# Performance work log

Hardware: AMD Instinct MI355X
Metric: run time of the kernel (lower is better)

Reference implementation:

```python
import jax, jax.numpy as jnp
import numpy as np

NUM_GRAPHS = 256
BN_EPS = 1e-5
GN_EPS = 1e-5


def setup_inputs() -> dict:
    key = jax.random.key(0)
    ks = jax.random.split(key, 8)
    N, E, D, H = 100000, 600000, 128, 128
    x = jax.random.normal(ks[0], (N, D), dtype=jnp.float32)
    W1 = jax.random.normal(ks[1], (4, 4 * H, D), dtype=jnp.float32) * 0.05
    bn_g = jnp.ones((4, 4 * H), dtype=jnp.float32)
    bn_b = jnp.zeros((4, 4 * H), dtype=jnp.float32)
    W2 = jax.random.normal(ks[2], (4, H, 4 * H), dtype=jnp.float32) * 0.05
    b2 = jnp.zeros((4, H), dtype=jnp.float32)
    gn_g = jnp.ones((4, H), dtype=jnp.float32)
    gn_b = jnp.zeros((4, H), dtype=jnp.float32)
    gn_a = jnp.ones((4, H), dtype=jnp.float32)
    edge_index = jax.random.randint(ks[3], (2, E), 0, N, dtype=jnp.int64)
    batch = jnp.sort(jax.random.randint(ks[4], (N,), 0, NUM_GRAPHS, dtype=jnp.int64))
    return {"x": x, "W1": W1, "bn_g": bn_g, "bn_b": bn_b, "W2": W2, "b2": b2,
            "gn_g": gn_g, "gn_b": gn_b, "gn_a": gn_a,
            "edge_index": edge_index, "batch": batch}


def reference(x, W1, bn_g, bn_b, W2, b2, gn_g, gn_b, gn_a, edge_index, batch):
    N = x.shape[0]
    src, dst = edge_index[0], edge_index[1]
    # per-graph node counts (shared by GraphNorm and mean-pool)
    cnt = jax.ops.segment_sum(jnp.ones((N,), x.dtype), batch, num_segments=NUM_GRAPHS)
    cnt = jnp.maximum(cnt, 1.0)[:, None]  # [G,1]

    h = x
    hs = []
    for l in range(4):  # fixed small layer loop
        # GINConv: (1+eps)*x + sum_{j->i} x_j, eps=0 default
        agg = jax.ops.segment_sum(h[src], dst, num_segments=N)
        z = h + agg
        # MLP: Linear(no bias) -> BatchNorm1d (batch stats) -> SELU -> Linear
        z = z @ W1[l].T
        mu = jnp.mean(z, axis=0)
        var = jnp.mean((z - mu) ** 2, axis=0)
        z = (z - mu) * jax.lax.rsqrt(var + BN_EPS) * bn_g[l] + bn_b[l]
        z = jax.nn.selu(z)
        z = z @ W2[l].T + b2[l]
        # GraphNorm: per-graph mean/var with learnable mean scale alpha
        gmean = jax.ops.segment_sum(z, batch, num_segments=NUM_GRAPHS) / cnt
        sub = z - gn_a[l] * gmean[batch]
        gvar = jax.ops.segment_sum(sub * sub, batch, num_segments=NUM_GRAPHS) / cnt
        z = gn_g[l] * sub * jax.lax.rsqrt(gvar[batch] + GN_EPS) + gn_b[l]
        z = jax.nn.selu(z)  # self.act (SELU, matching MLP)
        hs.append(z)
        h = z

    hg = jnp.concatenate(hs, axis=1)  # [N, 4*H]
    pooled = jax.ops.segment_sum(hg, batch, num_segments=NUM_GRAPHS) / cnt
    return pooled
```

## Files before the change

### kernel.cpp

```cpp
#include <hip/hip_runtime.h>
#include <hip/hip_bf16.h>


typedef __attribute__((ext_vector_type(8))) short bf16x8;
typedef __attribute__((ext_vector_type(4))) float f32x4;

#define MOMB 256

__device__ __forceinline__ unsigned short f2b(float x){
    __hip_bfloat16 h = __float2bfloat16(x);
    return *reinterpret_cast<unsigned short*>(&h);
}
__device__ __forceinline__ float b2f(unsigned short u){
    __hip_bfloat16 h;
    *reinterpret_cast<unsigned short*>(&h) = u;
    return __bfloat162float(h);
}
__device__ __forceinline__ float selu_f(float x){
    const float sc = 1.0507009873554805f, al = 1.6732632423543772f;
    return x > 0.f ? sc * x : sc * al * (__expf(x) - 1.f);
}

__global__ void count_kernel(const int* __restrict__ dst, int* __restrict__ counts, int E){
    int e = blockIdx.x * 256 + threadIdx.x;
    if (e < E) atomicAdd(&counts[dst[e]], 1);
}

__global__ void cnt_bs_kernel(const int* __restrict__ batch, float* __restrict__ cnt, int N){
    __shared__ int sb[257];
    int g = threadIdx.x;
    int lo = 0, hi = N;
    while (lo < hi){ int mid = (lo + hi) >> 1; if (batch[mid] < g) lo = mid + 1; else hi = mid; }
    sb[g] = lo;
    if (g == 0) sb[256] = N;
    __syncthreads();
    cnt[g] = fmaxf((float)(sb[g + 1] - sb[g]), 1.f);
}

__global__ __launch_bounds__(1024) void scan_kernel(const int* __restrict__ counts,
                                                    int* __restrict__ row_ptr, int N){
    __shared__ int wsum[16];
    __shared__ int wpre[16];
    __shared__ int s_total;
    __shared__ int s_running;
    int tid = threadIdx.x;
    int lane = tid & 63, wid = tid >> 6;
    if (tid == 0) s_running = 0;
    __syncthreads();
    for (int base = 0; base < N; base += 4096){
        int idx0 = base + tid * 4;
        int v[4];
        #pragma unroll
        for (int j = 0; j < 4; j++) v[j] = (idx0 + j < N) ? counts[idx0 + j] : 0;
        int tsum = v[0] + v[1] + v[2] + v[3];
        int x = tsum;
        #pragma unroll
        for (int off = 1; off < 64; off <<= 1){
            int y = __shfl_up(x, off, 64);
            if (lane >= off) x += y;
        }
        if (lane == 63) wsum[wid] = x;
        __syncthreads();
        if (wid == 0 && lane < 16){
            int w = wsum[lane];
            int xx = w;
            #pragma unroll
            for (int off = 1; off < 16; off <<= 1){
                int y = __shfl_up(xx, off, 64);
                if (lane >= off) xx += y;
            }
            wpre[lane] = xx - w;
            if (lane == 15) s_total = xx;
        }
        __syncthreads();
        int run = s_running + wpre[wid] + (x - tsum);
        #pragma unroll
        for (int j = 0; j < 4; j++){
            if (idx0 + j < N) row_ptr[idx0 + j] = run;
            run += v[j];
        }
        __syncthreads();
        if (tid == 0) s_running += s_total;
        __syncthreads();
    }
    if (tid == 0) row_ptr[N] = s_running;
}

__global__ void fill_kernel(const int* __restrict__ ei, const int* __restrict__ row_ptr,
                            int* __restrict__ fill, int* __restrict__ colv, int E){
    int e = blockIdx.x * 256 + threadIdx.x;
    if (e < E){
        int s = ei[e];
        int d = ei[E + e];
        int pos = atomicAdd(&fill[d], 1);
        colv[row_ptr[d] + pos] = s;
    }
}

__global__ void pack_kernel(const float* __restrict__ W1, const float* __restrict__ W2,
                            unsigned short* __restrict__ W1p, unsigned short* __restrict__ W2p){
    int t = blockIdx.x * 256 + threadIdx.x;
    int which = t >> 15;
    int u = t & 32767;
    int lane = u & 63; u >>= 6;
    int nf = u & 3; u >>= 2;
    int wc = u & 1; u >>= 1;
    int kk = u & 3; u >>= 2;
    int c = u & 3; u >>= 2;
    int l = u;
    int col = wc * 64 + nf * 16 + (lane & 15);
    int kbase = kk * 32 + (lane >> 4) * 8;
    size_t ob = ((((((size_t)(l * 4 + c) * 4 + kk) * 2 + wc) * 4 + nf) * 2) * 512) + lane * 8;
    unsigned short* dst = which == 0 ? W1p : W2p;
    #pragma unroll
    for (int j = 0; j < 8; j++){
        int k = kbase + j;
        float wv = which == 0 ? W1[((size_t)(l * 512) + c * 128 + col) * 128 + k]
                              : W2[((size_t)(l * 128) + col) * 512 + c * 128 + k];
        unsigned short hi = f2b(wv);
        unsigned short lo = f2b(wv - b2f(hi));
        dst[ob + j] = hi;
        dst[ob + 512 + j] = lo;
    }
}

__global__ __launch_bounds__(256) void agg_split_kernel(
    const float* __restrict__ h, const int* __restrict__ row_ptr,
    const int* __restrict__ colv,
    unsigned short* __restrict__ zhi, unsigned short* __restrict__ zlo, int N)
{
    int t = blockIdx.x * 256 + threadIdx.x;
    int i = t >> 5;
    if (i >= N) return;
    int vo = (t & 31);
    const float4* hv = reinterpret_cast<const float4*>(h);
    int p0 = row_ptr[i], p1 = row_ptr[i + 1];
    float4 acc = hv[(size_t)i * 32 + vo];
    int p = p0;
    for (; p + 4 <= p1; p += 4){
        int s0 = colv[p], s1 = colv[p + 1], s2 = colv[p + 2], s3 = colv[p + 3];
        float4 a = hv[(size_t)s0 * 32 + vo];
        float4 b = hv[(size_t)s1 * 32 + vo];
        float4 c = hv[(size_t)s2 * 32 + vo];
        float4 d = hv[(size_t)s3 * 32 + vo];
        acc.x += (a.x + b.x) + (c.x + d.x);
        acc.y += (a.y + b.y) + (c.y + d.y);
        acc.z += (a.z + b.z) + (c.z + d.z);
        acc.w += (a.w + b.w) + (c.w + d.w);
    }
    for (; p < p1; p++){
        float4 a = hv[(size_t)colv[p] * 32 + vo];
        acc.x += a.x; acc.y += a.y; acc.z += a.z; acc.w += a.w;
    }
    float vals[4] = {acc.x, acc.y, acc.z, acc.w};
    unsigned int h01, h23, l01, l23;
    {
        unsigned short hh[4], ll[4];
        #pragma unroll
        for (int j = 0; j < 4; j++){
            hh[j] = f2b(vals[j]);
            ll[j] = f2b(vals[j] - b2f(hh[j]));
        }
        h01 = (unsigned int)hh[0] | ((unsigned int)hh[1] << 16);
        h23 = (unsigned int)hh[2] | ((unsigned int)hh[3] << 16);
        l01 = (unsigned int)ll[0] | ((unsigned int)ll[1] << 16);
        l23 = (unsigned int)ll[2] | ((unsigned int)ll[3] << 16);
    }
    int kk = vo >> 3, kg = (vo >> 1) & 3, half = vo & 1;
    size_t fo = ((size_t)(i >> 4) * 4 + kk) * 512 + (kg * 16 + (i & 15)) * 8 + half * 4;
    *reinterpret_cast<uint2*>(zhi + fo) = make_uint2(h01, h23);
    *reinterpret_cast<uint2*>(zlo + fo) = make_uint2(l01, l23);
}

__device__ __forceinline__ bf16x8 tread(const unsigned short* __restrict__ s, int base){
    union { bf16x8 v; unsigned short u[8]; } r;
    #pragma unroll
    for (int j = 0; j < 8; j++) r.u[j] = s[base + j * 8];
    return r.v;
}

__global__ __launch_bounds__(256) void moment_k(
    const unsigned short* __restrict__ Zhi_g, const unsigned short* __restrict__ Zlo_g,
    float* __restrict__ Mpart, float* __restrict__ cpart, int RB)
{
    __shared__ __align__(16) unsigned short Zh_s[16384];
    __shared__ __align__(16) unsigned short Zl_s[16384];
    __shared__ float cs[256];
    int tid = threadIdx.x, lane = tid & 63, w = tid >> 6;
    int fl = lane & 15, g = lane >> 4;
    int tpart = (g >> 1) * 2048 + (g & 1) * 64;
    int fpart = (fl >> 3) * 128 + (fl & 7);

    f32x4 acc[2][8];
    #pragma unroll
    for (int i = 0; i < 2; i++)
        #pragma unroll
        for (int j = 0; j < 8; j++) acc[i][j] = (f32x4){0.f, 0.f, 0.f, 0.f};
    float csum = 0.f;
    int cf = tid & 127, chalf = tid >> 7;
    int cfbase = (cf >> 5) * 512 + ((cf >> 3) & 3) * 128 + (cf & 7);

    for (int blk = blockIdx.x; blk < RB; blk += MOMB){
        __syncthreads();
        {
            size_t gbase = (size_t)blk * 16384;
            const uint4* gh = reinterpret_cast<const uint4*>(Zhi_g + gbase);
            const uint4* gl = reinterpret_cast<const uint4*>(Zlo_g + gbase);
            uint4* sh4 = reinterpret_cast<uint4*>(Zh_s);
            uint4* sl4 = reinterpret_cast<uint4*>(Zl_s);
            #pragma unroll
            for (int j = 0; j < 8; j++){
                sh4[j * 256 + tid] = gh[j * 256 + tid];
                sl4[j * 256 + tid] = gl[j * 256 + tid];
            }
        }
        __syncthreads();

        #pragma unroll 8
        for (int n = chalf * 64; n < chalf * 64 + 64; n++){
            int addr = (n >> 4) * 2048 + (n & 15) * 8 + cfbase;
            csum += b2f(Zh_s[addr]) + b2f(Zl_s[addr]);
        }

        for (int nk = 0; nk < 4; nk++){
            int nb = nk * 4096 + tpart + fpart;
            bf16x8 ath[2], atl[2];
            #pragma unroll
            for (int i = 0; i < 2; i++){
                int ft = w * 2 + i;
                int base = nb + (ft >> 1) * 512 + (ft & 1) * 256;
                ath[i] = tread(Zh_s, base);
                atl[i] = tread(Zl_s, base);
            }
            #pragma unroll
            for (int ft2 = 0; ft2 < 8; ft2++){
                int base2 = nb + (ft2 >> 1) * 512 + (ft2 & 1) * 256;
                bf16x8 bth = tread(Zh_s, base2);
                bf16x8 btl = tread(Zl_s, base2);
                #pragma unroll
                for (int i = 0; i < 2; i++){
                    acc[i][ft2] = __builtin_amdgcn_mfma_f32_16x16x32_bf16(ath[i], bth, acc[i][ft2], 0, 0, 0);
                    acc[i][ft2] = __builtin_amdgcn_mfma_f32_16x16x32_bf16(ath[i], btl, acc[i][ft2], 0, 0, 0);
                    acc[i][ft2] = __builtin_amdgcn_mfma_f32_16x16x32_bf16(atl[i], bth, acc[i][ft2], 0, 0, 0);
                }
            }
        }
    }

    float* Mp = Mpart + (size_t)blockIdx.x * 16384;
    int col = lane & 15, rbase = (lane >> 4) * 4;
    #pragma unroll
    for (int i = 0; i < 2; i++)
        #pragma unroll
        for (int ft2 = 0; ft2 < 8; ft2++)
            #pragma unroll
            for (int r = 0; r < 4; r++){
                int a = (w * 2 + i) * 16 + rbase + r;
                int b = ft2 * 16 + col;
                Mp[a * 128 + b] = acc[i][ft2][r];
            }
    cs[tid] = csum;
    __syncthreads();
    if (tid < 128) cpart[(size_t)blockIdx.x * 128 + tid] = cs[tid] + cs[tid + 128];
}

__global__ __launch_bounds__(256) void reduce_k(
    const float* __restrict__ Mpart, const float* __restrict__ cpart,
    float* __restrict__ Msum, float* __restrict__ colsum)
{
    int gid = blockIdx.x * 256 + threadIdx.x;
    float s = 0.f;
    for (int p = 0; p < MOMB; p++) s += Mpart[(size_t)p * 16384 + gid];
    Msum[gid] = s;
    if (blockIdx.x == 0 && threadIdx.x < 128){
        float c = 0.f;
        for (int p = 0; p < MOMB; p++) c += cpart[(size_t)p * 128 + threadIdx.x];
        colsum[threadIdx.x] = c;
    }
}

__global__ __launch_bounds__(128) void bn_final2_k(
    const float* __restrict__ Msum, const float* __restrict__ colsum,
    const float* __restrict__ W1, const float* __restrict__ bng,
    const float* __restrict__ bnb, float* __restrict__ sc, float* __restrict__ sh,
    int l, float invN)
{
    __shared__ float s_w[128];
    __shared__ float red[4];
    int j = blockIdx.x;
    int t = threadIdx.x;
    float wt = W1[(size_t)l * 65536 + (size_t)j * 128 + t];
    s_w[t] = wt;
    __syncthreads();
    float y = 0.f;
    #pragma unroll 4
    for (int k = 0; k < 128; k++) y = fmaf(Msum[t * 128 + k], s_w[k], y);
    float p = wt * y;
    float mc = wt * colsum[t];
    #pragma unroll
    for (int off = 32; off >= 1; off >>= 1){
        p += __shfl_xor(p, off, 64);
        mc += __shfl_xor(mc, off, 64);
    }
    int lane = t & 63, wv = t >> 6;
    if (lane == 0){ red[wv * 2] = p; red[wv * 2 + 1] = mc; }
    __syncthreads();
    if (t == 0){
        float e2 = (red[0] + red[2]) * invN;
        float mu = (red[1] + red[3]) * invN;
        float var = e2 - mu * mu;
        float inv = rsqrtf(var + 1e-5f);
        float gg = bng[l * 512 + j] * inv;
        sc[j] = gg;
        sh[j] = bnb[l * 512 + j] - mu * gg;
    }
}

__global__ __launch_bounds__(512, 1) void fused_k(
    const unsigned short* __restrict__ Zhi_g, const unsigned short* __restrict__ Zlo_g,
    const unsigned short* __restrict__ B1p, const unsigned short* __restrict__ B2p,
    float* __restrict__ Z, const float* __restrict__ bsc, const float* __restrict__ bsh,
    const float* __restrict__ b2l, int N)
{
    __shared__ __align__(16) unsigned short Zh_s[16384];
    __shared__ __align__(16) unsigned short Zl_s[16384];
    __shared__ __align__(16) unsigned short Ph[128][136];
    __shared__ __align__(16) unsigned short Pl[128][136];
    __shared__ float s_sc[512], s_sh[512];
    int tid = threadIdx.x, lane = tid & 63, w = tid >> 6;
    int wr = w >> 2, wq = w & 3;
    int r_lo = lane & 15, kg = lane >> 4;
    int m0 = blockIdx.x * 128;

    if (tid < 512){ s_sc[tid] = bsc[tid]; s_sh[tid] = bsh[tid]; }
    {
        size_t gbase = (size_t)(m0 >> 4) * 2048;
        const uint4* gh = reinterpret_cast<const uint4*>(Zhi_g + gbase);
        const uint4* gl = reinterpret_cast<const uint4*>(Zlo_g + gbase);
        uint4* sh4 = reinterpret_cast<uint4*>(Zh_s);
        uint4* sl4 = reinterpret_cast<uint4*>(Zl_s);
        #pragma unroll
        for (int j = 0; j < 4; j++){
            sh4[j * 512 + tid] = gh[j * 512 + tid];
            sl4[j * 512 + tid] = gl[j * 512 + tid];
        }
    }
    __syncthreads();

    int wc = wq >> 1;
    f32x4 acc2[4][2];
    #pragma unroll
    for (int i = 0; i < 4; i++)
        #pragma unroll
        for (int j = 0; j < 2; j++) acc2[i][j] = (f32x4){0.f, 0.f, 0.f, 0.f};

    for (int c = 0; c < 4; c++){
        f32x4 acc1[2][4];
        #pragma unroll
        for (int i = 0; i < 2; i++)
            #pragma unroll
            for (int j = 0; j < 4; j++) acc1[i][j] = (f32x4){0.f, 0.f, 0.f, 0.f};

        const bf16x8* B1v = reinterpret_cast<const bf16x8*>(B1p) + (size_t)c * 4096;
        for (int kk = 0; kk < 4; kk++){
            bf16x8 awh[2], awl[2];
            #pragma unroll
            for (int mfp = 0; mfp < 2; mfp++){
                int colblk = wq * 2 + mfp;
                int wc1 = colblk >> 2, nf1 = colblk & 3;
                int ob = ((kk * 2 + wc1) * 4 + nf1) * 2;
                awh[mfp] = B1v[(ob + 0) * 64 + lane];
                awl[mfp] = B1v[(ob + 1) * 64 + lane];
            }
            bf16x8 bzh[4], bzl[4];
            #pragma unroll
            for (int nfp = 0; nfp < 4; nfp++){
                int so = ((wr * 4 + nfp) * 4 + kk) * 512 + lane * 8;
                bzh[nfp] = *reinterpret_cast<const bf16x8*>(&Zh_s[so]);
                bzl[nfp] = *reinterpret_cast<const bf16x8*>(&Zl_s[so]);
            }
            #pragma unroll
            for (int mfp = 0; mfp < 2; mfp++)
                #pragma unroll
                for (int nfp = 0; nfp < 4; nfp++){
                    acc1[mfp][nfp] = __builtin_amdgcn_mfma_f32_16x16x32_bf16(awh[mfp], bzh[nfp], acc1[mfp][nfp], 0, 0, 0);
                    acc1[mfp][nfp] = __builtin_amdgcn_mfma_f32_16x16x32_bf16(awh[mfp], bzl[nfp], acc1[mfp][nfp], 0, 0, 0);
                    acc1[mfp][nfp] = __builtin_amdgcn_mfma_f32_16x16x32_bf16(awl[mfp], bzh[nfp], acc1[mfp][nfp], 0, 0, 0);
                }
        }

        __syncthreads();
        #pragma unroll
        for (int mfp = 0; mfp < 2; mfp++){
            int ckb = wq * 32 + mfp * 16 + kg * 4;
            float sc0 = s_sc[c * 128 + ckb + 0], sh0 = s_sh[c * 128 + ckb + 0];
            float sc1 = s_sc[c * 128 + ckb + 1], sh1 = s_sh[c * 128 + ckb + 1];
            float sc2 = s_sc[c * 128 + ckb + 2], sh2 = s_sh[c * 128 + ckb + 2];
            float sc3 = s_sc[c * 128 + ckb + 3], sh3 = s_sh[c * 128 + ckb + 3];
            #pragma unroll
            for (int nfp = 0; nfp < 4; nfp++){
                float t0 = selu_f(fmaf(acc1[mfp][nfp][0], sc0, sh0));
                float t1 = selu_f(fmaf(acc1[mfp][nfp][1], sc1, sh1));
                float t2 = selu_f(fmaf(acc1[mfp][nfp][2], sc2, sh2));
                float t3 = selu_f(fmaf(acc1[mfp][nfp][3], sc3, sh3));
                unsigned short h0 = f2b(t0), h1 = f2b(t1), h2 = f2b(t2), h3 = f2b(t3);
                unsigned short l0 = f2b(t0 - b2f(h0)), l1 = f2b(t1 - b2f(h1));
                unsigned short l2 = f2b(t2 - b2f(h2)), l3 = f2b(t3 - b2f(h3));
                int node = wr * 64 + nfp * 16 + r_lo;
                uint2 hv = make_uint2((unsigned int)h0 | ((unsigned int)h1 << 16),
                                      (unsigned int)h2 | ((unsigned int)h3 << 16));
                uint2 lv = make_uint2((unsigned int)l0 | ((unsigned int)l1 << 16),
                                      (unsigned int)l2 | ((unsigned int)l3 << 16));
                *reinterpret_cast<uint2*>(&Ph[node][ckb]) = hv;
                *reinterpret_cast<uint2*>(&Pl[node][ckb]) = lv;
            }
        }
        __syncthreads();

        const bf16x8* B2v = reinterpret_cast<const bf16x8*>(B2p);
        for (int kk2 = 0; kk2 < 4; kk2++){
            int kkf = c * 4 + kk2;
            bf16x8 bh[2], bl[2];
            #pragma unroll
            for (int nf = 0; nf < 2; nf++){
                int nfold = (wq & 1) * 2 + nf;
                int ob = ((kkf * 2 + wc) * 4 + nfold) * 2;
                bh[nf] = B2v[(ob + 0) * 64 + lane];
                bl[nf] = B2v[(ob + 1) * 64 + lane];
            }
            bf16x8 ah[4], alr[4];
            #pragma unroll
            for (int mf = 0; mf < 4; mf++){
                int ar = wr * 64 + mf * 16 + r_lo;
                ah[mf]  = *reinterpret_cast<const bf16x8*>(&Ph[ar][kk2 * 32 + kg * 8]);
                alr[mf] = *reinterpret_cast<const bf16x8*>(&Pl[ar][kk2 * 32 + kg * 8]);
            }
            #pragma unroll
            for (int mf = 0; mf < 4; mf++)
                #pragma unroll
                for (int nf = 0; nf < 2; nf++){
                    acc2[mf][nf] = __builtin_amdgcn_mfma_f32_16x16x32_bf16(ah[mf],  bh[nf], acc2[mf][nf], 0, 0, 0);
                    acc2[mf][nf] = __builtin_amdgcn_mfma_f32_16x16x32_bf16(ah[mf],  bl[nf], acc2[mf][nf], 0, 0, 0);
                    acc2[mf][nf] = __builtin_amdgcn_mfma_f32_16x16x32_bf16(alr[mf], bh[nf], acc2[mf][nf], 0, 0, 0);
                }
        }
    }

    #pragma unroll
    for (int nf = 0; nf < 2; nf++){
        int col = wq * 32 + nf * 16 + r_lo;
        float bv = b2l[col];
        #pragma unroll
        for (int mf = 0; mf < 4; mf++)
            #pragma unroll
            for (int r = 0; r < 4; r++){
                int row = m0 + wr * 64 + mf * 16 + kg * 4 + r;
                if (row < N)
                    Z[(size_t)row * 128 + col] = bv + acc2[mf][nf][r];
            }
    }
}

__global__ __launch_bounds__(256) void gn_stats_kernel(
    const float* __restrict__ z2, const int* __restrict__ batch,
    float* __restrict__ gsum, float* __restrict__ gsq, int N)
{
    __shared__ int sb[128];
    int tid = threadIdx.x;
    int base = blockIdx.x * 128;
    int end = min(128, N - base);
    if (tid < 128) sb[tid] = (tid < end) ? batch[base + tid] : 0;
    __syncthreads();
    int vo = tid & 31;
    int r0 = (tid >> 5) * 16;
    if (r0 >= end) return;
    int rend = min(r0 + 16, end);
    const float4* zv = reinterpret_cast<const float4*>(z2);
    float sx = 0.f, sy = 0.f, sz = 0.f, sw = 0.f;
    float qx = 0.f, qy = 0.f, qz = 0.f, qw = 0.f;
    int run_g = sb[r0];
    for (int r = r0; r < rend; r++){
        int g = sb[r];
        if (g != run_g){
            float* gs = &gsum[run_g * 128 + vo * 4];
            float* gq = &gsq[run_g * 128 + vo * 4];
            atomicAdd(gs + 0, sx); atomicAdd(gs + 1, sy); atomicAdd(gs + 2, sz); atomicAdd(gs + 3, sw);
            atomicAdd(gq + 0, qx); atomicAdd(gq + 1, qy); atomicAdd(gq + 2, qz); atomicAdd(gq + 3, qw);
            sx = sy = sz = sw = 0.f; qx = qy = qz = qw = 0.f;
            run_g = g;
        }
        float4 v = zv[(size_t)(base + r) * 32 + vo];
        sx += v.x; sy += v.y; sz += v.z; sw += v.w;
        qx += v.x * v.x; qy += v.y * v.y; qz += v.z * v.z; qw += v.w * v.w;
    }
    float* gs = &gsum[run_g * 128 + vo * 4];
    float* gq = &gsq[run_g * 128 + vo * 4];
    atomicAdd(gs + 0, sx); atomicAdd(gs + 1, sy); atomicAdd(gs + 2, sz); atomicAdd(gs + 3, sw);
    atomicAdd(gq + 0, qx); atomicAdd(gq + 1, qy); atomicAdd(gq + 2, qz); atomicAdd(gq + 3, qw);
}

__global__ void gn_final_kernel(float* __restrict__ gsum, float* __restrict__ gsq,
                                const float* __restrict__ cnt,
                                const float* __restrict__ gng, const float* __restrict__ gnb,
                                const float* __restrict__ gna,
                                float* __restrict__ scale, float* __restrict__ shift, int l){
    int g = blockIdx.x, c = threadIdx.x;
    int idx = g * 128 + c;
    float n = cnt[g];
    float m = gsum[idx] / n;
    float e2 = gsq[idx] / n;
    float a = gna[l * 128 + c];
    float var = e2 - (2.f * a - a * a) * m * m;
    float inv = rsqrtf(var + 1e-5f);
    float sc = gng[l * 128 + c] * inv;
    scale[idx] = sc;
    shift[idx] = gnb[l * 128 + c] - a * m * sc;
    gsum[idx] = 0.f;
    gsq[idx] = 0.f;
}

__global__ __launch_bounds__(256) void gn_apply_kernel(
    float* __restrict__ z2h, const int* __restrict__ batch,
    const float* __restrict__ scale, const float* __restrict__ shift,
    float* __restrict__ pool, int l, int N)
{
    __shared__ int sb[128];
    int tid = threadIdx.x;
    int base = blockIdx.x * 128;
    int end = min(128, N - base);
    if (tid < 128) sb[tid] = (tid < end) ? batch[base + tid] : 0;
    __syncthreads();
    int vo = tid & 31;
    int r0 = (tid >> 5) * 16;
    if (r0 >= end) return;
    int rend = min(r0 + 16, end);
    float4* zv = reinterpret_cast<float4*>(z2h);
    int run_g = sb[r0];
    float scx = scale[run_g * 128 + vo * 4 + 0], shx = shift[run_g * 128 + vo * 4 + 0];
    float scy = scale[run_g * 128 + vo * 4 + 1], shy = shift[run_g * 128 + vo * 4 + 1];
    float scz = scale[run_g * 128 + vo * 4 + 2], shz = shift[run_g * 128 + vo * 4 + 2];
    float scw = scale[run_g * 128 + vo * 4 + 3], shw = shift[run_g * 128 + vo * 4 + 3];
    float px = 0.f, py = 0.f, pz = 0.f, pw = 0.f;
    for (int r = r0; r < rend; r++){
        int g = sb[r];
        if (g != run_g){
            float* pp = &pool[run_g * 512 + l * 128 + vo * 4];
            atomicAdd(pp + 0, px); atomicAdd(pp + 1, py); atomicAdd(pp + 2, pz); atomicAdd(pp + 3, pw);
            px = py = pz = pw = 0.f;
            run_g = g;
            scx = scale[g * 128 + vo * 4 + 0]; shx = shift[g * 128 + vo * 4 + 0];
            scy = scale[g * 128 + vo * 4 + 1]; shy = shift[g * 128 + vo * 4 + 1];
            scz = scale[g * 128 + vo * 4 + 2]; shz = shift[g * 128 + vo * 4 + 2];
            scw = scale[g * 128 + vo * 4 + 3]; shw = shift[g * 128 + vo * 4 + 3];
        }
        size_t idx = (size_t)(base + r) * 32 + vo;
        float4 v = zv[idx];
        v.x = selu_f(fmaf(v.x, scx, shx));
        v.y = selu_f(fmaf(v.y, scy, shy));
        v.z = selu_f(fmaf(v.z, scz, shz));
        v.w = selu_f(fmaf(v.w, scw, shw));
        zv[idx] = v;
        px += v.x; py += v.y; pz += v.z; pw += v.w;
    }
    float* pp = &pool[run_g * 512 + l * 128 + vo * 4];
    atomicAdd(pp + 0, px); atomicAdd(pp + 1, py); atomicAdd(pp + 2, pz); atomicAdd(pp + 3, pw);
}

__global__ void final_kernel(const float* __restrict__ pool, const float* __restrict__ cnt,
                             float* __restrict__ out, int n){
    int i = blockIdx.x * 256 + threadIdx.x;
    if (i < n) out[i] = pool[i] / cnt[i >> 9];
}

extern "C" void kernel_launch(void* const* d_in, const int* in_sizes, int n_in,
                              void* d_out, int out_size, void* d_ws, size_t ws_size,
                              hipStream_t stream){
    const float* x    = (const float*)d_in[0];
    const float* W1   = (const float*)d_in[1];
    const float* bng  = (const float*)d_in[2];
    const float* bnb  = (const float*)d_in[3];
    const float* W2   = (const float*)d_in[4];
    const float* b2   = (const float*)d_in[5];
    const float* gng  = (const float*)d_in[6];
    const float* gnb  = (const float*)d_in[7];
    const float* gna  = (const float*)d_in[8];
    const int*   ei   = (const int*)d_in[9];
    const int*   batch= (const int*)d_in[10];
    int N = in_sizes[0] / 128;
    int E = in_sizes[9] / 2;
    float* out = (float*)d_out;
    int RB = (N + 127) / 128;

    char* ws = (char*)d_ws;
    size_t off = 0;
    auto alloc = [&](size_t bytes) -> char* {
        char* p = ws + off;
        off += (bytes + 255) & ~(size_t)255;
        return p;
    };
    unsigned short* z0hi = (unsigned short*)alloc((size_t)RB * 128 * 128 * 2);
    unsigned short* z0lo = (unsigned short*)alloc((size_t)RB * 128 * 128 * 2);
    float* z2     = (float*)alloc((size_t)N * 128 * 4);
    unsigned short* W1p = (unsigned short*)alloc(524288 * 2);
    unsigned short* W2p = (unsigned short*)alloc(524288 * 2);
    int*   row_ptr= (int*)alloc((size_t)(N + 1) * 4);
    int*   colv   = (int*)alloc((size_t)E * 4);
    int*   counts = (int*)alloc((size_t)N * 4);
    int*   fill   = (int*)alloc((size_t)N * 4);
    float* cnt_f  = (float*)alloc(256 * 4);
    float* Mpart  = (float*)alloc((size_t)MOMB * 16384 * 4);
    float* cpart  = (float*)alloc((size_t)MOMB * 128 * 4);
    float* Msum   = (float*)alloc(16384 * 4);
    float* colsum = (float*)alloc(128 * 4);
    float* bn_sc  = (float*)alloc(512 * 4);
    float* bn_sh  = (float*)alloc(512 * 4);
    float* gn_sum = (float*)alloc(256 * 128 * 4);
    float* gn_sq  = (float*)alloc(256 * 128 * 4);
    float* gn_sc  = (float*)alloc(256 * 128 * 4);
    float* gn_sh  = (float*)alloc(256 * 128 * 4);
    float* pool   = (float*)alloc(256 * 512 * 4);
    (void)ws_size;

    hipMemsetAsync(counts, 0, (size_t)N * 4, stream);
    hipMemsetAsync(fill,   0, (size_t)N * 4, stream);
    hipMemsetAsync(gn_sum, 0, 2 * 256 * 128 * 4, stream);
    hipMemsetAsync(pool,   0, 256 * 512 * 4, stream);
    {
        size_t tail_start = (size_t)(N >> 4) * 2048;
        size_t total      = (size_t)RB * 128 * 128;
        if (total > tail_start){
            size_t tail_bytes = (total - tail_start) * 2;
            hipMemsetAsync(z0hi + tail_start, 0, tail_bytes, stream);
            hipMemsetAsync(z0lo + tail_start, 0, tail_bytes, stream);
        }
    }

    pack_kernel<<<256, 256, 0, stream>>>(W1, W2, W1p, W2p);
    count_kernel<<<(E + 255) / 256, 256, 0, stream>>>(ei + E, counts, E);
    scan_kernel<<<1, 1024, 0, stream>>>(counts, row_ptr, N);
    fill_kernel<<<(E + 255) / 256, 256, 0, stream>>>(ei, row_ptr, fill, colv, E);
    cnt_bs_kernel<<<1, 256, 0, stream>>>(batch, cnt_f, N);

    const float* hcur = x;
    float invN = 1.f / (float)N;
    for (int l = 0; l < 4; l++){
        agg_split_kernel<<<(N + 7) / 8, 256, 0, stream>>>(hcur, row_ptr, colv, z0hi, z0lo, N);
        moment_k<<<MOMB, 256, 0, stream>>>(z0hi, z0lo, Mpart, cpart, RB);
        reduce_k<<<64, 256, 0, stream>>>(Mpart, cpart, Msum, colsum);
        bn_final2_k<<<512, 128, 0, stream>>>(Msum, colsum, W1, bng, bnb,
                                             bn_sc, bn_sh, l, invN);
        fused_k<<<RB, 512, 0, stream>>>(z0hi, z0lo, W1p + (size_t)l * 131072,
                                        W2p + (size_t)l * 131072, z2,
                                        bn_sc, bn_sh, b2 + l * 128, N);
        gn_stats_kernel<<<RB, 256, 0, stream>>>(z2, batch, gn_sum, gn_sq, N);
        gn_final_kernel<<<256, 128, 0, stream>>>(gn_sum, gn_sq, cnt_f, gng, gnb, gna,
                                                 gn_sc, gn_sh, l);
        gn_apply_kernel<<<RB, 256, 0, stream>>>(z2, batch, gn_sc, gn_sh, pool, l, N);
        hcur = z2;
    }
    final_kernel<<<(out_size + 255) / 256, 256, 0, stream>>>(pool, cnt_f, out, out_size);
}
```

Baseline: 1.475 ms.

## Fuse GraphNorm stats into fused MLP kernel and use 1024-thread blocks

Removes the separate gn_stats kernel by accumulating per-graph sum and sum-of-squares in the fused MLP epilogue, using run-length segments over the sorted batch ids, which saves re-reading z2 from memory. It also doubles the block to 1024 threads (16 waves), halving each wave's node tile so per-thread accumulator registers drop. The tradeoff is more atomics: each output column now issues them per small run instead of per larger run. Register pressure under launch_bounds(1024,1) may also cause spills.

```diff
diff --git a/kernel.cpp b/kernel.cpp
--- a/kernel.cpp
+++ b/kernel.cpp
@@ -316,23 +316,26 @@
     }
 }
 
-__global__ __launch_bounds__(512, 1) void fused_k(
+__global__ __launch_bounds__(1024, 1) void fused_k(
     const unsigned short* __restrict__ Zhi_g, const unsigned short* __restrict__ Zlo_g,
     const unsigned short* __restrict__ B1p, const unsigned short* __restrict__ B2p,
     float* __restrict__ Z, const float* __restrict__ bsc, const float* __restrict__ bsh,
-    const float* __restrict__ b2l, int N)
+    const float* __restrict__ b2l, const int* __restrict__ batch,
+    float* __restrict__ gsum, float* __restrict__ gsq, int N)
 {
     __shared__ __align__(16) unsigned short Zh_s[16384];
     __shared__ __align__(16) unsigned short Zl_s[16384];
     __shared__ __align__(16) unsigned short Ph[128][136];
     __shared__ __align__(16) unsigned short Pl[128][136];
     __shared__ float s_sc[512], s_sh[512];
+    __shared__ int s_b[128];
     int tid = threadIdx.x, lane = tid & 63, w = tid >> 6;
     int wr = w >> 2, wq = w & 3;
     int r_lo = lane & 15, kg = lane >> 4;
     int m0 = blockIdx.x * 128;
 
     if (tid < 512){ s_sc[tid] = bsc[tid]; s_sh[tid] = bsh[tid]; }
+    if (tid < 128) s_b[tid] = (m0 + tid < N) ? batch[m0 + tid] : -1;
     {
         size_t gbase = (size_t)(m0 >> 4) * 2048;
         const uint4* gh = reinterpret_cast<const uint4*>(Zhi_g + gbase);
@@ -340,26 +343,26 @@
         uint4* sh4 = reinterpret_cast<uint4*>(Zh_s);
         uint4* sl4 = reinterpret_cast<uint4*>(Zl_s);
         #pragma unroll
-        for (int j = 0; j < 4; j++){
-            sh4[j * 512 + tid] = gh[j * 512 + tid];
-            sl4[j * 512 + tid] = gl[j * 512 + tid];
+        for (int j = 0; j < 2; j++){
+            sh4[j * 1024 + tid] = gh[j * 1024 + tid];
+            sl4[j * 1024 + tid] = gl[j * 1024 + tid];
         }
     }
     __syncthreads();
 
     int wc = wq >> 1;
-    f32x4 acc2[4][2];
+    f32x4 acc2[2][2];
     #pragma unroll
-    for (int i = 0; i < 4; i++)
+    for (int i = 0; i < 2; i++)
         #pragma unroll
         for (int j = 0; j < 2; j++) acc2[i][j] = (f32x4){0.f, 0.f, 0.f, 0.f};
 
     for (int c = 0; c < 4; c++){
-        f32x4 acc1[2][4];
+        f32x4 acc1[2][2];
         #pragma unroll
         for (int i = 0; i < 2; i++)
             #pragma unroll
-            for (int j = 0; j < 4; j++) acc1[i][j] = (f32x4){0.f, 0.f, 0.f, 0.f};
+            for (int j = 0; j < 2; j++) acc1[i][j] = (f32x4){0.f, 0.f, 0.f, 0.f};
 
         const bf16x8* B1v = reinterpret_cast<const bf16x8*>(B1p) + (size_t)c * 4096;
         for (int kk = 0; kk < 4; kk++){
@@ -372,17 +375,17 @@
                 awh[mfp] = B1v[(ob + 0) * 64 + lane];
                 awl[mfp] = B1v[(ob + 1) * 64 + lane];
             }
-            bf16x8 bzh[4], bzl[4];
-            #pragma unroll
-            for (int nfp = 0; nfp < 4; nfp++){
-                int so = ((wr * 4 + nfp) * 4 + kk) * 512 + lane * 8;
+            bf16x8 bzh[2], bzl[2];
+            #pragma unroll
+            for (int nfp = 0; nfp < 2; nfp++){
+                int so = (((wr * 2 + nfp) * 4) + kk) * 512 + lane * 8;
                 bzh[nfp] = *reinterpret_cast<const bf16x8*>(&Zh_s[so]);
                 bzl[nfp] = *reinterpret_cast<const bf16x8*>(&Zl_s[so]);
             }
             #pragma unroll
             for (int mfp = 0; mfp < 2; mfp++)
                 #pragma unroll
-                for (int nfp = 0; nfp < 4; nfp++){
+                for (int nfp = 0; nfp < 2; nfp++){
                     acc1[mfp][nfp] = __builtin_amdgcn_mfma_f32_16x16x32_bf16(awh[mfp], bzh[nfp], acc1[mfp][nfp], 0, 0, 0);
                     acc1[mfp][nfp] = __builtin_amdgcn_mfma_f32_16x16x32_bf16(awh[mfp], bzl[nfp], acc1[mfp][nfp], 0, 0, 0);
                     acc1[mfp][nfp] = __builtin_amdgcn_mfma_f32_16x16x32_bf16(awl[mfp], bzh[nfp], acc1[mfp][nfp], 0, 0, 0);
@@ -398,7 +401,7 @@
             float sc2 = s_sc[c * 128 + ckb + 2], sh2 = s_sh[c * 128 + ckb + 2];
             float sc3 = s_sc[c * 128 + ckb + 3], sh3 = s_sh[c * 128 + ckb + 3];
             #pragma unroll
-            for (int nfp = 0; nfp < 4; nfp++){
+            for (int nfp = 0; nfp < 2; nfp++){
                 float t0 = selu_f(fmaf(acc1[mfp][nfp][0], sc0, sh0));
                 float t1 = selu_f(fmaf(acc1[mfp][nfp][1], sc1, sh1));
                 float t2 = selu_f(fmaf(acc1[mfp][nfp][2], sc2, sh2));
@@ -406,7 +409,7 @@
                 unsigned short h0 = f2b(t0), h1 = f2b(t1), h2 = f2b(t2), h3 = f2b(t3);
                 unsigned short l0 = f2b(t0 - b2f(h0)), l1 = f2b(t1 - b2f(h1));
                 unsigned short l2 = f2b(t2 - b2f(h2)), l3 = f2b(t3 - b2f(h3));
-                int node = wr * 64 + nfp * 16 + r_lo;
+                int node = wr * 32 + nfp * 16 + r_lo;
                 uint2 hv = make_uint2((unsigned int)h0 | ((unsigned int)h1 << 16),
                                       (unsigned int)h2 | ((unsigned int)h3 << 16));
                 uint2 lv = make_uint2((unsigned int)l0 | ((unsigned int)l1 << 16),
@@ -428,15 +431,15 @@
                 bh[nf] = B2v[(ob + 0) * 64 + lane];
                 bl[nf] = B2v[(ob + 1) * 64 + lane];
             }
-            bf16x8 ah[4], alr[4];
-            #pragma unroll
-            for (int mf = 0; mf < 4; mf++){
-                int ar = wr * 64 + mf * 16 + r_lo;
+            bf16x8 ah[2], alr[2];
+            #pragma unroll
+            for (int mf = 0; mf < 2; mf++){
+                int ar = wr * 32 + mf * 16 + r_lo;
                 ah[mf]  = *reinterpret_cast<const bf16x8*>(&Ph[ar][kk2 * 32 + kg * 8]);
                 alr[mf] = *reinterpret_cast<const bf16x8*>(&Pl[ar][kk2 * 32 + kg * 8]);
             }
             #pragma unroll
-            for (int mf = 0; mf < 4; mf++)
+            for (int mf = 0; mf < 2; mf++)
                 #pragma unroll
                 for (int nf = 0; nf < 2; nf++){
                     acc2[mf][nf] = __builtin_amdgcn_mfma_f32_16x16x32_bf16(ah[mf],  bh[nf], acc2[mf][nf], 0, 0, 0);
@@ -450,53 +453,33 @@
     for (int nf = 0; nf < 2; nf++){
         int col = wq * 32 + nf * 16 + r_lo;
         float bv = b2l[col];
-        #pragma unroll
-        for (int mf = 0; mf < 4; mf++)
+        float s = 0.f, q = 0.f;
+        int run_g = -2;
+        #pragma unroll
+        for (int mf = 0; mf < 2; mf++)
             #pragma unroll
             for (int r = 0; r < 4; r++){
-                int row = m0 + wr * 64 + mf * 16 + kg * 4 + r;
-                if (row < N)
-                    Z[(size_t)row * 128 + col] = bv + acc2[mf][nf][r];
-            }
-    }
-}
-
-__global__ __launch_bounds__(256) void gn_stats_kernel(
-    const float* __restrict__ z2, const int* __restrict__ batch,
-    float* __restrict__ gsum, float* __restrict__ gsq, int N)
-{
-    __shared__ int sb[128];
-    int tid = threadIdx.x;
-    int base = blockIdx.x * 128;
-    int end = min(128, N - base);
-    if (tid < 128) sb[tid] = (tid < end) ? batch[base + tid] : 0;
-    __syncthreads();
-    int vo = tid & 31;
-    int r0 = (tid >> 5) * 16;
-    if (r0 >= end) return;
-    int rend = min(r0 + 16, end);
-    const float4* zv = reinterpret_cast<const float4*>(z2);
-    float sx = 0.f, sy = 0.f, sz = 0.f, sw = 0.f;
-    float qx = 0.f, qy = 0.f, qz = 0.f, qw = 0.f;
-    int run_g = sb[r0];
-    for (int r = r0; r < rend; r++){
-        int g = sb[r];
-        if (g != run_g){
-            float* gs = &gsum[run_g * 128 + vo * 4];
-            float* gq = &gsq[run_g * 128 + vo * 4];
-            atomicAdd(gs + 0, sx); atomicAdd(gs + 1, sy); atomicAdd(gs + 2, sz); atomicAdd(gs + 3, sw);
-            atomicAdd(gq + 0, qx); atomicAdd(gq + 1, qy); atomicAdd(gq + 2, qz); atomicAdd(gq + 3, qw);
-            sx = sy = sz = sw = 0.f; qx = qy = qz = qw = 0.f;
-            run_g = g;
-        }
-        float4 v = zv[(size_t)(base + r) * 32 + vo];
-        sx += v.x; sy += v.y; sz += v.z; sw += v.w;
-        qx += v.x * v.x; qy += v.y * v.y; qz += v.z * v.z; qw += v.w * v.w;
-    }
-    float* gs = &gsum[run_g * 128 + vo * 4];
-    float* gq = &gsq[run_g * 128 + vo * 4];
-    atomicAdd(gs + 0, sx); atomicAdd(gs + 1, sy); atomicAdd(gs + 2, sz); atomicAdd(gs + 3, sw);
-    atomicAdd(gq + 0, qx); atomicAdd(gq + 1, qy); atomicAdd(gq + 2, qz); atomicAdd(gq + 3, qw);
+                int row_l = wr * 32 + mf * 16 + kg * 4 + r;
+                int row = m0 + row_l;
+                if (row < N){
+                    float v = bv + acc2[mf][nf][r];
+                    Z[(size_t)row * 128 + col] = v;
+                    int g = s_b[row_l];
+                    if (g != run_g){
+                        if (run_g >= 0){
+                            atomicAdd(&gsum[run_g * 128 + col], s);
+                            atomicAdd(&gsq[run_g * 128 + col], q);
+                        }
+                        s = 0.f; q = 0.f; run_g = g;
+                    }
+                    s += v; q += v * v;
+                }
+            }
+        if (run_g >= 0){
+            atomicAdd(&gsum[run_g * 128 + col], s);
+            atomicAdd(&gsq[run_g * 128 + col], q);
+        }
+    }
 }
 
 __global__ void gn_final_kernel(float* __restrict__ gsum, float* __restrict__ gsq,
@@ -649,10 +632,10 @@
         reduce_k<<<64, 256, 0, stream>>>(Mpart, cpart, Msum, colsum);
         bn_final2_k<<<512, 128, 0, stream>>>(Msum, colsum, W1, bng, bnb,
                                              bn_sc, bn_sh, l, invN);
-        fused_k<<<RB, 512, 0, stream>>>(z0hi, z0lo, W1p + (size_t)l * 131072,
-                                        W2p + (size_t)l * 131072, z2,
-                                        bn_sc, bn_sh, b2 + l * 128, N);
-        gn_stats_kernel<<<RB, 256, 0, stream>>>(z2, batch, gn_sum, gn_sq, N);
+        fused_k<<<RB, 1024, 0, stream>>>(z0hi, z0lo, W1p + (size_t)l * 131072,
+                                         W2p + (size_t)l * 131072, z2,
+                                         bn_sc, bn_sh, b2 + l * 128,
+                                         batch, gn_sum, gn_sq, N);
         gn_final_kernel<<<256, 128, 0, stream>>>(gn_sum, gn_sq, cnt_f, gng, gnb, gna,
                                                  gn_sc, gn_sh, l);
         gn_apply_kernel<<<RB, 256, 0, stream>>>(z2, batch, gn_sc, gn_sh, pool, l, N);
```

After: 1.395 ms. 5.4% less time.
